# Optimization experiments

Measured on AMD Instinct MI355X. Metric: run time of the kernel, lower is better.

Reference implementation:

```python
import jax, jax.numpy as jnp
import numpy as np

EPS = float(np.finfo(np.float32).eps)
SEQ_LEN = 2048
NUM_HEADS = 16
DIM_EMB = 1024
DIM_HEAD = DIM_EMB // NUM_HEADS
DIM_K = DIM_EMB  # module scales by full dim_k, not per-head dim
BATCH = 2


def cosine_positional_encoding(seq_len, dim):
    idx = jnp.arange(seq_len, dtype=jnp.float32)
    scale = 1.0 / (10000.0 ** (jnp.arange(0, dim, 2, dtype=jnp.float32) / dim) + EPS)
    ang = idx[:, None] * scale[None, :]  # [S, dim/2]
    # interleave sin (even) and cos (odd) along last dim -> [S, dim]
    return jnp.stack([jnp.sin(ang), jnp.cos(ang)], axis=-1).reshape(seq_len, dim)


def setup_inputs() -> dict:
    key = jax.random.key(0)
    ks = jax.random.split(key, 5)
    s = DIM_EMB ** -0.5
    return {
        "x": jax.random.normal(ks[0], (BATCH, SEQ_LEN, DIM_EMB), dtype=jnp.float32),
        "Wq": jax.random.normal(ks[1], (DIM_EMB, DIM_EMB), dtype=jnp.float32) * s,
        "Wk": jax.random.normal(ks[2], (DIM_EMB, DIM_EMB), dtype=jnp.float32) * s,
        "Wv": jax.random.normal(ks[3], (DIM_EMB, DIM_EMB), dtype=jnp.float32) * s,
        "Wo": jax.random.normal(ks[4], (DIM_EMB, DIM_EMB), dtype=jnp.float32) * s,
    }


def reference(x, Wq, Wk, Wv, Wo):
    B, S, E = x.shape
    pos = cosine_positional_encoding(S, DIM_HEAD)  # [S, dim_head]
    # projections (bias-free)
    def split_heads(t):
        return t.reshape(B, S, NUM_HEADS, DIM_HEAD).transpose(0, 2, 1, 3)  # [B,H,S,D]
    q = split_heads(x @ Wq) + pos[None, None]
    k = split_heads(x @ Wk) + pos[None, None]
    v = split_heads(x @ Wv)
    scores = jnp.einsum("bhqd,bhkd->bhqk", q, k) * (DIM_K ** -0.5)
    causal_mask = jnp.triu(jnp.ones((S, S), dtype=bool), k=1)
    m_inf = -jnp.finfo(scores.dtype).max
    scores = jnp.where(causal_mask[None, None], m_inf, scores)
    attn = jax.nn.softmax(scores, axis=-1)
    out = jnp.einsum("bhqk,bhkd->bhqd", attn, v)
    out = out.transpose(0, 2, 1, 3).reshape(B, S, E)
    return out @ Wo
```

## Files before the change

kernel.cpp:

```cpp
#include <hip/hip_runtime.h>
#include <math.h>

#define BATCH 2
#define SEQ   2048
#define EMB   1024
#define NHEAD 16
#define DHEAD 64
#define MROWS (BATCH*SEQ)
#define QKVS  3072

typedef unsigned int  uint;
typedef unsigned short ushort;
typedef __attribute__((ext_vector_type(8))) short short8;
typedef __attribute__((ext_vector_type(4))) float f32x4;

__device__ __forceinline__ float exp2_fast(float x) {
    return __builtin_amdgcn_exp2f(x);
}

__global__ void pos_init(float* __restrict__ pos) {
    int s = blockIdx.x;
    int d = threadIdx.x;
    int i = d >> 1;
    float expo  = (float)(2 * i) / (float)DHEAD;
    float scale = 1.0f / (powf(10000.0f, expo) + 1.1920928955078125e-07f);
    float ang   = (float)s * scale;
    pos[s * DHEAD + d] = (d & 1) ? cosf(ang) : sinf(ang);
}

__device__ __forceinline__ uint pack_bf16x2(float a, float b) {
    union { float f; uint u; } x, y;
    x.f = a; y.f = b;
    uint ua = x.u + 0x7fffu + ((x.u >> 16) & 1u);
    uint ub = y.u + 0x7fffu + ((y.u >> 16) & 1u);
    return (ua >> 16) | (ub & 0xffff0000u);
}
__device__ __forceinline__ ushort bf16_1(float a) {
    union { float f; uint u; } x; x.f = a;
    return (ushort)((x.u + 0x7fffu + ((x.u >> 16) & 1u)) >> 16);
}

__device__ __forceinline__ void gll16(const ushort* g, ushort* l) {
    __builtin_amdgcn_global_load_lds(
        (const __attribute__((address_space(1))) uint*)g,
        (__attribute__((address_space(3))) uint*)l, 16, 0, 0);
}

__global__ __launch_bounds__(256) void cvt_bf16(
    const float* __restrict__ in, ushort* __restrict__ out, int n2) {
    int gid = blockIdx.x * 256 + threadIdx.x;
    if (gid < n2) {
        float2 v = ((const float2*)in)[gid];
        ((uint*)out)[gid] = pack_bf16x2(v.x, v.y);
    }
}

__global__ __launch_bounds__(256) void wt_bf16_all(
    const float* __restrict__ Wq, const float* __restrict__ Wk,
    const float* __restrict__ Wv, const float* __restrict__ Wo,
    ushort* __restrict__ Wqkvt, ushort* __restrict__ Wot) {
    __shared__ float tile[32][33];
    const int which = blockIdx.z;
    const float* W = (which == 0) ? Wq : (which == 1) ? Wk : (which == 2) ? Wv : Wo;
    ushort* Wt = (which < 3) ? (Wqkvt + (size_t)which * 1024 * EMB) : Wot;
    const int c0 = blockIdx.x * 32;
    const int r0 = blockIdx.y * 32;
    const int tx = threadIdx.x & 31;
    const int ty = threadIdx.x >> 5;
#pragma unroll
    for (int i = 0; i < 4; ++i)
        tile[ty + i * 8][tx] = W[(size_t)(r0 + ty + i * 8) * EMB + c0 + tx];
    __syncthreads();
#pragma unroll
    for (int i = 0; i < 4; ++i)
        Wt[(size_t)(c0 + ty + i * 8) * EMB + r0 + tx] = bf16_1(tile[tx][ty + i * 8]);
}

__global__ __launch_bounds__(256) void vt_tr(
    const ushort* __restrict__ QKV, ushort* __restrict__ Vt) {
    __shared__ ushort tile[64][72];
    const int s0 = blockIdx.x * 64;
    const int bh = blockIdx.y;
    const int b  = bh >> 4, h = bh & 15;
    const int t  = threadIdx.x;
    const int r  = t >> 2;
    const int c  = (t & 3) * 16;
    const ushort* src = QKV + (size_t)(b * SEQ + s0 + r) * QKVS + 2048 + h * 64 + c;
    *(uint4*)&tile[r][c]     = *(const uint4*)src;
    *(uint4*)&tile[r][c + 8] = *(const uint4*)(src + 8);
    __syncthreads();
    uint ov[8];
#pragma unroll
    for (int i = 0; i < 8; ++i) {
        uint lo = tile[c + 2 * i][r];
        uint hi = tile[c + 2 * i + 1][r];
        ov[i] = lo | (hi << 16);
    }
    ushort* dst = Vt + ((size_t)bh * 64 + r) * SEQ + s0 + c;
    *(uint4*)dst       = *(uint4*)&ov[0];
    *(uint4*)(dst + 8) = *(uint4*)&ov[4];
}

#define TM 128
#define TN 128
#define TK 32

__global__ __launch_bounds__(256) void gemm_mfma2(
    const ushort* __restrict__ A, const ushort* __restrict__ Bt,
    void* __restrict__ Cv, const float* __restrict__ pos, int posmode,
    int out_bf16, int N, int K) {
    __shared__ ushort As[TM * TK];
    __shared__ ushort Bs[TN * TK];

    const int t    = threadIdx.x;
    const int lane = t & 63, w = t >> 6;
    const int quad = lane >> 4, l15 = lane & 15;
    const int bm = blockIdx.x * TM, bn = blockIdx.y * TN;
    const int wm = (w & 1) * 64, wn = (w >> 1) * 64;
    const int r0 = t >> 2, kp = (t & 3) * 8;

    f32x4 acc[4][4];
#pragma unroll
    for (int mi = 0; mi < 4; ++mi)
#pragma unroll
        for (int ni = 0; ni < 4; ++ni)
            acc[mi][ni] = (f32x4){0.f, 0.f, 0.f, 0.f};

    const ushort* Ap0 = A  + (size_t)(bm + r0) * K + kp;
    const ushort* Ap1 = A  + (size_t)(bm + 64 + r0) * K + kp;
    const ushort* Bp0 = Bt + (size_t)(bn + r0) * K + kp;
    const ushort* Bp1 = Bt + (size_t)(bn + 64 + r0) * K + kp;
    ushort* Asd0 = &As[t * 8];
    ushort* Asd1 = &As[2048 + t * 8];
    ushort* Bsd0 = &Bs[t * 8];
    ushort* Bsd1 = &Bs[2048 + t * 8];

    for (int k0 = 0; k0 < K; k0 += TK) {
        __syncthreads();
        gll16(Ap0 + k0, Asd0);
        gll16(Ap1 + k0, Asd1);
        gll16(Bp0 + k0, Bsd0);
        gll16(Bp1 + k0, Bsd1);
        __syncthreads();

        short8 af[4], bfv[4];
#pragma unroll
        for (int mi = 0; mi < 4; ++mi)
            af[mi] = *(const short8*)&As[(wm + mi * 16 + l15) * TK + quad * 8];
#pragma unroll
        for (int ni = 0; ni < 4; ++ni)
            bfv[ni] = *(const short8*)&Bs[(wn + ni * 16 + l15) * TK + quad * 8];
#pragma unroll
        for (int mi = 0; mi < 4; ++mi)
#pragma unroll
            for (int ni = 0; ni < 4; ++ni)
                acc[mi][ni] = __builtin_amdgcn_mfma_f32_16x16x32_bf16(
                    af[mi], bfv[ni], acc[mi][ni], 0, 0, 0);
    }

#pragma unroll
    for (int mi = 0; mi < 4; ++mi) {
#pragma unroll
        for (int r = 0; r < 4; ++r) {
            const int row = bm + wm + mi * 16 + quad * 4 + r;
            const int s   = row & (SEQ - 1);
#pragma unroll
            for (int ni = 0; ni < 4; ++ni) {
                const int col = bn + wn + ni * 16 + l15;
                float v = acc[mi][ni][r];
                if (posmode && col < 2048) v += pos[s * DHEAD + (col & 63)];
                if (out_bf16) ((ushort*)Cv)[(size_t)row * N + col] = bf16_1(v);
                else          ((float*) Cv)[(size_t)row * N + col] = v;
            }
        }
    }
}

#define LDP 72

__global__ __launch_bounds__(256) void attn_mfma3(
    const ushort* __restrict__ QKV, const ushort* __restrict__ Vt,
    ushort* __restrict__ AOb) {
    __shared__ ushort Ks[64 * LDP];
    __shared__ ushort Vs[64 * LDP];
    __shared__ ushort Ps[64 * LDP];

    const int pair = blockIdx.x;
    const int bh   = blockIdx.y;
    const int b    = bh >> 4, h = bh & 15;
    const int t    = threadIdx.x;
    const int lane = t & 63, w = t >> 6;
    const int quad = lane >> 4, l15 = lane & 15;
    const int wrow = w * 16;
    const int sr = t >> 2;
    const int sc = (t & 3) * 16;
    const float SCL = 0.03125f * 1.44269504088896f;

    const size_t qbase = (size_t)b * SEQ * QKVS + h * 64;
    const ushort* kpb = QKV + qbase + 1024 + (size_t)sr * QKVS + sc;
    const ushort* vpb = Vt + ((size_t)bh * 64 + sr) * SEQ;

#pragma unroll
    for (int ph = 0; ph < 2; ++ph) {
        const int qt = ph ? (31 - pair) : pair;

        const ushort* qp = QKV + qbase + (size_t)(qt * 64 + wrow + l15) * QKVS + quad * 8;
        const short8 aq0 = *(const short8*)qp;
        const short8 aq1 = *(const short8*)(qp + 32);

        uint4 ka = *(const uint4*)kpb;
        uint4 kb = *(const uint4*)(kpb + 8);
        uint4 va = *(const uint4*)(vpb + sc);
        uint4 vb = *(const uint4*)(vpb + sc + 8);

        f32x4 acc_o[4];
#pragma unroll
        for (int nd = 0; nd < 4; ++nd) acc_o[nd] = (f32x4){0.f, 0.f, 0.f, 0.f};
        float m_l = -3.0e38f, l_l = 0.f;
        const int qrow_g = qt * 64 + wrow + l15;

        for (int kt = 0; kt <= qt; ++kt) {
            __syncthreads();
            *(uint4*)&Ks[sr * LDP + sc]     = ka;
            *(uint4*)&Ks[sr * LDP + sc + 8] = kb;
            *(uint4*)&Vs[sr * LDP + sc]     = va;
            *(uint4*)&Vs[sr * LDP + sc + 8] = vb;
            const int ktn = (kt < qt) ? kt + 1 : qt;
            ka = *(const uint4*)(kpb + (size_t)ktn * 64 * QKVS);
            kb = *(const uint4*)(kpb + (size_t)ktn * 64 * QKVS + 8);
            va = *(const uint4*)(vpb + ktn * 64 + sc);
            vb = *(const uint4*)(vpb + ktn * 64 + sc + 8);
            __syncthreads();

            float sv[4][4];
            float mloc = m_l;
            const bool diag = (kt == qt);
#pragma unroll
            for (int kg = 0; kg < 4; ++kg) {
                const short8 ak0 = *(const short8*)&Ks[(kg * 16 + l15) * LDP + quad * 8];
                const short8 ak1 = *(const short8*)&Ks[(kg * 16 + l15) * LDP + 32 + quad * 8];
                f32x4 a = (f32x4){0.f, 0.f, 0.f, 0.f};
                a = __builtin_amdgcn_mfma_f32_16x16x32_bf16(ak0, aq0, a, 0, 0, 0);
                a = __builtin_amdgcn_mfma_f32_16x16x32_bf16(ak1, aq1, a, 0, 0, 0);
                const int keyb = kt * 64 + kg * 16 + quad * 4;
#pragma unroll
                for (int r = 0; r < 4; ++r) {
                    float v = a[r] * SCL;
                    if (diag && (keyb + r > qrow_g)) v = -3.0e38f;
                    sv[kg][r] = v;
                    mloc = fmaxf(mloc, v);
                }
            }
            mloc = fmaxf(mloc, __shfl_xor(mloc, 16, 64));
            mloc = fmaxf(mloc, __shfl_xor(mloc, 32, 64));
            const float alpha = exp2_fast(m_l - mloc);
            m_l = mloc;
            float rs = 0.f;
#pragma unroll
            for (int kg = 0; kg < 4; ++kg)
#pragma unroll
                for (int r = 0; r < 4; ++r) {
                    float p = exp2_fast(sv[kg][r] - mloc);
                    sv[kg][r] = p;
                    rs += p;
                }
            rs += __shfl_xor(rs, 16, 64);
            rs += __shfl_xor(rs, 32, 64);
            l_l = l_l * alpha + rs;

            float av[4];
#pragma unroll
            for (int r = 0; r < 4; ++r) av[r] = __shfl(alpha, quad * 4 + r, 64);
#pragma unroll
            for (int nd = 0; nd < 4; ++nd)
#pragma unroll
                for (int r = 0; r < 4; ++r) acc_o[nd][r] *= av[r];

#pragma unroll
            for (int kg = 0; kg < 4; ++kg) {
                uint2 u;
                u.x = pack_bf16x2(sv[kg][0], sv[kg][1]);
                u.y = pack_bf16x2(sv[kg][2], sv[kg][3]);
                *(uint2*)&Ps[(wrow + l15) * LDP + kg * 16 + quad * 4] = u;
            }
            const short8 pa0 = *(const short8*)&Ps[(wrow + l15) * LDP + quad * 8];
            const short8 pa1 = *(const short8*)&Ps[(wrow + l15) * LDP + 32 + quad * 8];
#pragma unroll
            for (int nd = 0; nd < 4; ++nd) {
                const short8 bv0 = *(const short8*)&Vs[(nd * 16 + l15) * LDP + quad * 8];
                const short8 bv1 = *(const short8*)&Vs[(nd * 16 + l15) * LDP + 32 + quad * 8];
                acc_o[nd] = __builtin_amdgcn_mfma_f32_16x16x32_bf16(pa0, bv0, acc_o[nd], 0, 0, 0);
                acc_o[nd] = __builtin_amdgcn_mfma_f32_16x16x32_bf16(pa1, bv1, acc_o[nd], 0, 0, 0);
            }
        }

        float linv[4];
#pragma unroll
        for (int r = 0; r < 4; ++r) linv[r] = 1.0f / __shfl(l_l, quad * 4 + r, 64);
#pragma unroll
        for (int nd = 0; nd < 4; ++nd)
#pragma unroll
            for (int r = 0; r < 4; ++r) {
                const int row = qt * 64 + wrow + quad * 4 + r;
                AOb[(size_t)(b * SEQ + row) * EMB + h * 64 + nd * 16 + l15] =
                    bf16_1(acc_o[nd][r] * linv[r]);
            }
    }
}

#define BM 64
#define BN 64
#define BK 16

__global__ __launch_bounds__(256) void gemm_f32(
    const float* __restrict__ A, const float* __restrict__ B,
    float* __restrict__ C, const float* __restrict__ pos, int addpos,
    int M, int N, int K) {
    __shared__ float As[BK][BM];
    __shared__ float Bs[BK][BN];
    const int tid = threadIdx.x;
    const int bm  = blockIdx.x * BM;
    const int bn  = blockIdx.y * BN;
    const int tx  = tid & 15;
    const int ty  = tid >> 4;
    const int arow = tid >> 2;
    const int acol = (tid & 3) << 2;
    const int brow = tid >> 4;
    const int bcol = (tid & 15) << 2;
    float acc[4][4] = {{0.f}};
    const float* Aptr = A + (size_t)(bm + arow) * K + acol;
    const float* Bptr = B + (size_t)brow * N + bn + bcol;
    for (int k0 = 0; k0 < K; k0 += BK) {
        float4 av = *(const float4*)(Aptr + k0);
        float4 bv = *(const float4*)(Bptr + (size_t)k0 * N);
        __syncthreads();
        As[acol + 0][arow] = av.x;
        As[acol + 1][arow] = av.y;
        As[acol + 2][arow] = av.z;
        As[acol + 3][arow] = av.w;
        *(float4*)&Bs[brow][bcol] = bv;
        __syncthreads();
#pragma unroll
        for (int kk = 0; kk < BK; ++kk) {
            float4 a = *(const float4*)&As[kk][ty << 2];
            float4 b = *(const float4*)&Bs[kk][tx << 2];
            float aa[4] = {a.x, a.y, a.z, a.w};
            float bb[4] = {b.x, b.y, b.z, b.w};
#pragma unroll
            for (int i = 0; i < 4; ++i)
#pragma unroll
                for (int j = 0; j < 4; ++j)
                    acc[i][j] += aa[i] * bb[j];
        }
    }
#pragma unroll
    for (int i = 0; i < 4; ++i) {
        int m = bm + (ty << 2) + i;
        int n = bn + (tx << 2);
        float4 v = make_float4(acc[i][0], acc[i][1], acc[i][2], acc[i][3]);
        if (addpos) {
            int s = m & (SEQ - 1);
            int d = n & (DHEAD - 1);
            float4 p = *(const float4*)&pos[s * DHEAD + d];
            v.x += p.x; v.y += p.y; v.z += p.z; v.w += p.w;
        }
        *(float4*)&C[(size_t)m * N + n] = v;
    }
}

#define QT 128
#define KT 32
__global__ __launch_bounds__(QT) void attn_fwd(
    const float* __restrict__ Q, const float* __restrict__ Kg,
    const float* __restrict__ V, float* __restrict__ O) {
    __shared__ float Ks[KT][DHEAD];
    __shared__ float Vs[KT][DHEAD];
    const int t    = threadIdx.x;
    const int q0   = blockIdx.x * QT;
    const int bh   = blockIdx.y;
    const int b    = bh >> 4;
    const int h    = bh & 15;
    const int qrow = q0 + t;
    const size_t base = (size_t)b * SEQ * EMB + (size_t)h * DHEAD;
    float4 q4[16], o4[16];
#pragma unroll
    for (int i = 0; i < 16; ++i) {
        q4[i] = *(const float4*)&Q[base + (size_t)qrow * EMB + i * 4];
        o4[i] = make_float4(0.f, 0.f, 0.f, 0.f);
    }
    float m_i = -3.0e38f, l_i = 0.0f;
    const float scale = 0.03125f;
    const int kend = q0 + QT;
    for (int k0 = 0; k0 < kend; k0 += KT) {
        __syncthreads();
#pragma unroll
        for (int i = 0; i < 4; ++i) {
            int idx = t + i * QT;
            int r = idx >> 4;
            int c = (idx & 15) << 2;
            *(float4*)&Ks[r][c] = *(const float4*)&Kg[base + (size_t)(k0 + r) * EMB + c];
            *(float4*)&Vs[r][c] = *(const float4*)&V [base + (size_t)(k0 + r) * EMB + c];
        }
        __syncthreads();
        float sv[KT];
        float mt = m_i;
#pragma unroll
        for (int j = 0; j < KT; ++j) {
            const float4* kr = (const float4*)Ks[j];
            float dot = 0.f;
#pragma unroll
            for (int dd = 0; dd < 16; ++dd) {
                float4 kv = kr[dd];
                dot += q4[dd].x * kv.x + q4[dd].y * kv.y +
                       q4[dd].z * kv.z + q4[dd].w * kv.w;
            }
            sv[j] = (k0 + j <= qrow) ? dot * scale : -3.0e38f;
            mt = fmaxf(mt, sv[j]);
        }
        float corr = __expf(m_i - mt);
        l_i *= corr;
#pragma unroll
        for (int i = 0; i < 16; ++i) {
            o4[i].x *= corr; o4[i].y *= corr; o4[i].z *= corr; o4[i].w *= corr;
        }
#pragma unroll
        for (int j = 0; j < KT; ++j) {
            float pp = __expf(sv[j] - mt);
            l_i += pp;
            const float4* vr = (const float4*)Vs[j];
#pragma unroll
            for (int dd = 0; dd < 16; ++dd) {
                float4 vv = vr[dd];
                o4[dd].x += pp * vv.x; o4[dd].y += pp * vv.y;
                o4[dd].z += pp * vv.z; o4[dd].w += pp * vv.w;
            }
        }
        m_i = mt;
    }
    float inv = 1.0f / l_i;
#pragma unroll
    for (int i = 0; i < 16; ++i) {
        float4 v = o4[i];
        v.x *= inv; v.y *= inv; v.z *= inv; v.w *= inv;
        *(float4*)&O[base + (size_t)qrow * EMB + i * 4] = v;
    }
}

extern "C" void kernel_launch(void* const* d_in, const int* in_sizes, int n_in,
                              void* d_out, int out_size, void* d_ws, size_t ws_size,
                              hipStream_t stream) {
    const float* x  = (const float*)d_in[0];
    const float* Wq = (const float*)d_in[1];
    const float* Wk = (const float*)d_in[2];
    const float* Wv = (const float*)d_in[3];
    const float* Wo = (const float*)d_in[4];
    float* out = (float*)d_out;

    char* ws = (char*)d_ws;
    size_t off = 0;
    float*  pos   = (float*)(ws + off);  off += (size_t)SEQ * DHEAD * 4;
    ushort* xb    = (ushort*)(ws + off); off += (size_t)MROWS * EMB * 2;
    ushort* Wqkvt = (ushort*)(ws + off); off += (size_t)QKVS * EMB * 2;
    ushort* Wot   = (ushort*)(ws + off); off += (size_t)EMB * EMB * 2;
    ushort* QKV   = (ushort*)(ws + off); off += (size_t)MROWS * QKVS * 2;
    ushort* Vtp   = (ushort*)(ws + off); off += (size_t)MROWS * EMB * 2;
    ushort* AOb   = (ushort*)(ws + off); off += (size_t)MROWS * EMB * 2;
    const bool use_bf16 = off <= ws_size;

    const int M = MROWS, K = EMB;

    pos_init<<<SEQ, DHEAD, 0, stream>>>(pos);

    if (use_bf16) {
        const int n2 = MROWS * EMB / 2;
        cvt_bf16<<<n2 / 256, 256, 0, stream>>>(x, xb, n2);
        wt_bf16_all<<<dim3(EMB / 32, EMB / 32, 4), 256, 0, stream>>>(
            Wq, Wk, Wv, Wo, Wqkvt, Wot);

        gemm_mfma2<<<dim3(M / TM, QKVS / TN), 256, 0, stream>>>(
            xb, Wqkvt, QKV, pos, 1, 1, QKVS, K);

        vt_tr<<<dim3(SEQ / 64, BATCH * NHEAD), 256, 0, stream>>>(QKV, Vtp);

        attn_mfma3<<<dim3(16, BATCH * NHEAD), 256, 0, stream>>>(QKV, Vtp, AOb);

        gemm_mfma2<<<dim3(M / TM, EMB / TN), 256, 0, stream>>>(
            AOb, Wot, out, pos, 0, 0, EMB, K);
    } else {
        size_t f = 0;
        float* posf = (float*)(ws + f); f += (size_t)SEQ * DHEAD * 4;
        float* Qb = (float*)(ws + f); f += (size_t)MROWS * EMB * 4;
        float* Kb = (float*)(ws + f); f += (size_t)MROWS * EMB * 4;
        float* Vb = (float*)(ws + f); f += (size_t)MROWS * EMB * 4;
        float* AO = (float*)(ws + f);
        dim3 g(M / BM, EMB / BN);
        gemm_f32<<<g, 256, 0, stream>>>(x, Wq, Qb, posf, 1, M, EMB, K);
        gemm_f32<<<g, 256, 0, stream>>>(x, Wk, Kb, posf, 1, M, EMB, K);
        gemm_f32<<<g, 256, 0, stream>>>(x, Wv, Vb, posf, 0, M, EMB, K);
        attn_fwd<<<dim3(SEQ / QT, BATCH * NHEAD), QT, 0, stream>>>(Qb, Kb, Vb, AO);
        gemm_f32<<<g, 256, 0, stream>>>(AO, Wo, out, posf, 0, M, EMB, K);
    }
}
```

Baseline: 218.5 us.

## Make attention waves independent with direct K/V fragment loads and prescaled Q

The attention kernel now gives each wave its own 16-row query chunk, paired causally across two phases. Each wave loads K and V MFMA fragments straight from global memory instead of staging shared tiles behind block-wide barriers, which removes the two __syncthreads per key tile and lets waves run skewed. The softmax scale (with log2e) is folded into the Q projection epilogue, and the causal mask is applied only on diagonal tiles. The grid is transposed so head varies fastest. The cost is redundant global or L2 traffic, since every wave re-reads K and V instead of sharing a staged tile, and Q is rounded to bf16 after scaling.

```diff
diff --git a/kernel.cpp b/kernel.cpp
--- a/kernel.cpp
+++ b/kernel.cpp
@@ -104,6 +104,7 @@
 #define TM 128
 #define TN 128
 #define TK 32
+#define SCLQ (0.03125f * 1.44269504088896f)
 
 __global__ __launch_bounds__(256) void gemm_mfma2(
     const ushort* __restrict__ A, const ushort* __restrict__ Bt,
@@ -168,7 +169,10 @@
             for (int ni = 0; ni < 4; ++ni) {
                 const int col = bn + wn + ni * 16 + l15;
                 float v = acc[mi][ni][r];
-                if (posmode && col < 2048) v += pos[s * DHEAD + (col & 63)];
+                if (posmode) {
+                    if (col < 2048) v += pos[s * DHEAD + (col & 63)];
+                    if (col < 1024) v *= SCLQ;
+                }
                 if (out_bf16) ((ushort*)Cv)[(size_t)row * N + col] = bf16_1(v);
                 else          ((float*) Cv)[(size_t)row * N + col] = v;
             }
@@ -176,79 +180,80 @@
     }
 }
 
-#define LDP 72
-
-__global__ __launch_bounds__(256) void attn_mfma3(
+#define LDPW 72
+
+__global__ __launch_bounds__(256) void attn_mfma4(
     const ushort* __restrict__ QKV, const ushort* __restrict__ Vt,
     ushort* __restrict__ AOb) {
-    __shared__ ushort Ks[64 * LDP];
-    __shared__ ushort Vs[64 * LDP];
-    __shared__ ushort Ps[64 * LDP];
-
-    const int pair = blockIdx.x;
-    const int bh   = blockIdx.y;
+    __shared__ ushort Ps[4 * 16 * LDPW];
+
+    const int bh   = blockIdx.x;
     const int b    = bh >> 4, h = bh & 15;
     const int t    = threadIdx.x;
     const int lane = t & 63, w = t >> 6;
     const int quad = lane >> 4, l15 = lane & 15;
-    const int wrow = w * 16;
-    const int sr = t >> 2;
-    const int sc = (t & 3) * 16;
-    const float SCL = 0.03125f * 1.44269504088896f;
+    ushort* Pw = &Ps[w * 16 * LDPW];
 
     const size_t qbase = (size_t)b * SEQ * QKVS + h * 64;
-    const ushort* kpb = QKV + qbase + 1024 + (size_t)sr * QKVS + sc;
-    const ushort* vpb = Vt + ((size_t)bh * 64 + sr) * SEQ;
+    const ushort* Kbp = QKV + qbase + 1024;
+    const ushort* Vbp = Vt + (size_t)bh * 64 * SEQ;
+
+    const int p = blockIdx.y * 4 + w;
 
 #pragma unroll
     for (int ph = 0; ph < 2; ++ph) {
-        const int qt = ph ? (31 - pair) : pair;
-
-        const ushort* qp = QKV + qbase + (size_t)(qt * 64 + wrow + l15) * QKVS + quad * 8;
-        const short8 aq0 = *(const short8*)qp;
-        const short8 aq1 = *(const short8*)(qp + 32);
-
-        uint4 ka = *(const uint4*)kpb;
-        uint4 kb = *(const uint4*)(kpb + 8);
-        uint4 va = *(const uint4*)(vpb + sc);
-        uint4 vb = *(const uint4*)(vpb + sc + 8);
+        const int c = ph ? (127 - p) : p;
+
+        const ushort* qp = QKV + qbase + (size_t)(c * 16 + l15) * QKVS + quad * 8;
+        const short8 bq0 = *(const short8*)qp;
+        const short8 bq1 = *(const short8*)(qp + 32);
 
         f32x4 acc_o[4];
 #pragma unroll
         for (int nd = 0; nd < 4; ++nd) acc_o[nd] = (f32x4){0.f, 0.f, 0.f, 0.f};
         float m_l = -3.0e38f, l_l = 0.f;
-        const int qrow_g = qt * 64 + wrow + l15;
-
-        for (int kt = 0; kt <= qt; ++kt) {
-            __syncthreads();
-            *(uint4*)&Ks[sr * LDP + sc]     = ka;
-            *(uint4*)&Ks[sr * LDP + sc + 8] = kb;
-            *(uint4*)&Vs[sr * LDP + sc]     = va;
-            *(uint4*)&Vs[sr * LDP + sc + 8] = vb;
-            const int ktn = (kt < qt) ? kt + 1 : qt;
-            ka = *(const uint4*)(kpb + (size_t)ktn * 64 * QKVS);
-            kb = *(const uint4*)(kpb + (size_t)ktn * 64 * QKVS + 8);
-            va = *(const uint4*)(vpb + ktn * 64 + sc);
-            vb = *(const uint4*)(vpb + ktn * 64 + sc + 8);
-            __syncthreads();
+        const int qrow = c * 16 + l15;
+        const int ktl  = c >> 2;
+
+        for (int kt = 0; kt <= ktl; ++kt) {
+            const bool diag = (kt == ktl);
+
+            short8 ak[4][2];
+#pragma unroll
+            for (int kg = 0; kg < 4; ++kg) {
+                const ushort* kp = Kbp + (size_t)(kt * 64 + kg * 16 + l15) * QKVS + quad * 8;
+                ak[kg][0] = *(const short8*)kp;
+                ak[kg][1] = *(const short8*)(kp + 32);
+            }
+            short8 bv[4][2];
+#pragma unroll
+            for (int nd = 0; nd < 4; ++nd) {
+                const ushort* vp = Vbp + (size_t)(nd * 16 + l15) * SEQ + kt * 64 + quad * 8;
+                bv[nd][0] = *(const short8*)vp;
+                bv[nd][1] = *(const short8*)(vp + 32);
+            }
 
             float sv[4][4];
             float mloc = m_l;
-            const bool diag = (kt == qt);
 #pragma unroll
             for (int kg = 0; kg < 4; ++kg) {
-                const short8 ak0 = *(const short8*)&Ks[(kg * 16 + l15) * LDP + quad * 8];
-                const short8 ak1 = *(const short8*)&Ks[(kg * 16 + l15) * LDP + 32 + quad * 8];
                 f32x4 a = (f32x4){0.f, 0.f, 0.f, 0.f};
-                a = __builtin_amdgcn_mfma_f32_16x16x32_bf16(ak0, aq0, a, 0, 0, 0);
-                a = __builtin_amdgcn_mfma_f32_16x16x32_bf16(ak1, aq1, a, 0, 0, 0);
-                const int keyb = kt * 64 + kg * 16 + quad * 4;
-#pragma unroll
-                for (int r = 0; r < 4; ++r) {
-                    float v = a[r] * SCL;
-                    if (diag && (keyb + r > qrow_g)) v = -3.0e38f;
-                    sv[kg][r] = v;
-                    mloc = fmaxf(mloc, v);
+                a = __builtin_amdgcn_mfma_f32_16x16x32_bf16(ak[kg][0], bq0, a, 0, 0, 0);
+                a = __builtin_amdgcn_mfma_f32_16x16x32_bf16(ak[kg][1], bq1, a, 0, 0, 0);
+                if (diag) {
+                    const int keyb = kt * 64 + kg * 16 + quad * 4;
+#pragma unroll
+                    for (int r = 0; r < 4; ++r) {
+                        float v = (keyb + r > qrow) ? -3.0e38f : a[r];
+                        sv[kg][r] = v;
+                        mloc = fmaxf(mloc, v);
+                    }
+                } else {
+#pragma unroll
+                    for (int r = 0; r < 4; ++r) {
+                        sv[kg][r] = a[r];
+                        mloc = fmaxf(mloc, a[r]);
+                    }
                 }
             }
             mloc = fmaxf(mloc, __shfl_xor(mloc, 16, 64));
@@ -260,9 +265,9 @@
             for (int kg = 0; kg < 4; ++kg)
 #pragma unroll
                 for (int r = 0; r < 4; ++r) {
-                    float p = exp2_fast(sv[kg][r] - mloc);
-                    sv[kg][r] = p;
-                    rs += p;
+                    float pv = exp2_fast(sv[kg][r] - mloc);
+                    sv[kg][r] = pv;
+                    rs += pv;
                 }
             rs += __shfl_xor(rs, 16, 64);
             rs += __shfl_xor(rs, 32, 64);
@@ -281,16 +286,14 @@
                 uint2 u;
                 u.x = pack_bf16x2(sv[kg][0], sv[kg][1]);
                 u.y = pack_bf16x2(sv[kg][2], sv[kg][3]);
-                *(uint2*)&Ps[(wrow + l15) * LDP + kg * 16 + quad * 4] = u;
-            }
-            const short8 pa0 = *(const short8*)&Ps[(wrow + l15) * LDP + quad * 8];
-            const short8 pa1 = *(const short8*)&Ps[(wrow + l15) * LDP + 32 + quad * 8];
+                *(uint2*)&Pw[l15 * LDPW + kg * 16 + quad * 4] = u;
+            }
+            const short8 pa0 = *(const short8*)&Pw[l15 * LDPW + quad * 8];
+            const short8 pa1 = *(const short8*)&Pw[l15 * LDPW + 32 + quad * 8];
 #pragma unroll
             for (int nd = 0; nd < 4; ++nd) {
-                const short8 bv0 = *(const short8*)&Vs[(nd * 16 + l15) * LDP + quad * 8];
-                const short8 bv1 = *(const short8*)&Vs[(nd * 16 + l15) * LDP + 32 + quad * 8];
-                acc_o[nd] = __builtin_amdgcn_mfma_f32_16x16x32_bf16(pa0, bv0, acc_o[nd], 0, 0, 0);
-                acc_o[nd] = __builtin_amdgcn_mfma_f32_16x16x32_bf16(pa1, bv1, acc_o[nd], 0, 0, 0);
+                acc_o[nd] = __builtin_amdgcn_mfma_f32_16x16x32_bf16(pa0, bv[nd][0], acc_o[nd], 0, 0, 0);
+                acc_o[nd] = __builtin_amdgcn_mfma_f32_16x16x32_bf16(pa1, bv[nd][1], acc_o[nd], 0, 0, 0);
             }
         }
 
@@ -301,7 +304,7 @@
         for (int nd = 0; nd < 4; ++nd)
 #pragma unroll
             for (int r = 0; r < 4; ++r) {
-                const int row = qt * 64 + wrow + quad * 4 + r;
+                const int row = c * 16 + quad * 4 + r;
                 AOb[(size_t)(b * SEQ + row) * EMB + h * 64 + nd * 16 + l15] =
                     bf16_1(acc_o[nd][r] * linv[r]);
             }
@@ -482,7 +485,7 @@
 
         vt_tr<<<dim3(SEQ / 64, BATCH * NHEAD), 256, 0, stream>>>(QKV, Vtp);
 
-        attn_mfma3<<<dim3(16, BATCH * NHEAD), 256, 0, stream>>>(QKV, Vtp, AOb);
+        attn_mfma4<<<dim3(BATCH * NHEAD, 16), 256, 0, stream>>>(QKV, Vtp, AOb);
 
         gemm_mfma2<<<dim3(M / TM, EMB / TN), 256, 0, stream>>>(
             AOb, Wot, out, pos, 0, 0, EMB, K);
```

Result: slower. 287.1 us (+31.4%).
